# Kernel optimization log

Measured on AMD Instinct MI355X. Metric: run time of the kernel, lower is better.

Reference implementation:

```python
import jax, jax.numpy as jnp
import numpy as np

B, S, D = 2, 512, 1024
H, DH = 16, 64
P, K, F = 16, 4, 4096
EPS = 1e-6


def setup_inputs() -> dict:
    key = jax.random.key(0)
    ks = jax.random.split(key, 9)
    sc = D ** -0.5
    return {
        "x": jax.random.normal(ks[0], (B, S, D), jnp.float32),
        "wq": jax.random.normal(ks[1], (D, D), jnp.float32) * sc,
        "wk": jax.random.normal(ks[2], (D, D), jnp.float32) * sc,
        "wv": jax.random.normal(ks[3], (D, D), jnp.float32) * sc,
        "wo": jax.random.normal(ks[4], (D, D), jnp.float32) * sc,
        "g1": jnp.ones((D,), jnp.float32),
        "g2": jnp.ones((D,), jnp.float32),
        "r1": jax.random.normal(ks[5], (D, P), jnp.float32) * sc,
        "r2": jax.random.normal(ks[6], (D, P), jnp.float32) * sc,
        "bank1": jax.random.normal(ks[7], (P, D, F), jnp.float32) * 0.02,
        "bank2": jax.random.normal(ks[8], (P, F, D), jnp.float32) * 0.02,
    }


def _rmsnorm(t, g):
    return t * jax.lax.rsqrt(jnp.mean(t * t, axis=-1, keepdims=True) + EPS) * g


def reference(x, wq, wk, wv, wo, g1, g2, r1, r2, bank1, bank2):
    # --- attention sublayer (pre-norm, causal SDPA) ---
    h = _rmsnorm(x, g1)
    q = (h @ wq).reshape(B, S, H, DH).transpose(0, 2, 1, 3)  # (B,H,S,DH)
    k = (h @ wk).reshape(B, S, H, DH).transpose(0, 2, 1, 3)
    v = (h @ wv).reshape(B, S, H, DH).transpose(0, 2, 1, 3)
    scores = jnp.einsum("bhqd,bhkd->bhqk", q, k) * (DH ** -0.5)
    causal = jnp.triu(jnp.ones((S, S), bool), k=1)
    scores = jnp.where(causal[None, None], jnp.finfo(scores.dtype).min, scores)
    attn = jax.nn.softmax(scores, axis=-1)
    o = jnp.einsum("bhqk,bhkd->bhqd", attn, v).transpose(0, 2, 1, 3).reshape(B, S, D)
    x = x + o @ wo

    # --- compositional FFN: top-k primitive-bank routing ---
    h = _rmsnorm(x, g2)
    # FC1 routing
    tv1, ti1 = jax.lax.top_k(h @ r1, K)            # (B,S,K)
    c1 = jax.nn.softmax(tv1, axis=-1)
    z1 = jnp.einsum("bsd,pdf->bspf", h, bank1)     # all-primitive FC1 projections
    z1k = jnp.take_along_axis(z1, ti1[..., None], axis=2)  # gather (B,S,K,F)
    hmid = jax.nn.gelu(jnp.einsum("bsk,bskf->bsf", c1, z1k))
    # FC2 routing (same pre-FFN features)
    tv2, ti2 = jax.lax.top_k(h @ r2, K)
    c2 = jax.nn.softmax(tv2, axis=-1)
    z2 = jnp.einsum("bsf,pfd->bspd", hmid, bank2)
    z2k = jnp.take_along_axis(z2, ti2[..., None], axis=2)  # (B,S,K,D)
    ffn_out = jnp.einsum("bsk,bskd->bsd", c2, z2k)
    return x + ffn_out
```

## Files before the change

### kernel.cpp

```cpp
#include <hip/hip_runtime.h>
#include <hip/hip_bf16.h>

#define B_  2
#define S_  512
#define D_  1024
#define H_  16
#define DH_ 64
#define P_  16
#define K_  4
#define F_  4096
#define NT  (B_*S_)
#define EPS_ 1e-6f
#define MT  6

typedef __attribute__((ext_vector_type(8))) short bf16x8s;
typedef __attribute__((ext_vector_type(4))) float f32x4;

__device__ inline unsigned short f2bf(float f) {
    unsigned int u = __builtin_bit_cast(unsigned int, f);
    unsigned int r = (u + 0x7fffu + ((u >> 16) & 1u)) >> 16;
    return (unsigned short)r;
}
__device__ inline float bf2f(unsigned short u) {
    unsigned int x = ((unsigned int)u) << 16;
    return __builtin_bit_cast(float, x);
}

__global__ void rmsnorm_kernel(const float* __restrict__ x, const float* __restrict__ g,
                               float* __restrict__ out, __hip_bfloat16* __restrict__ outbf) {
    int t = blockIdx.x;
    const float* row = x + (size_t)t * D_;
    float ss = 0.f;
    for (int d = threadIdx.x; d < D_; d += 256) { float v = row[d]; ss += v * v; }
    __shared__ float red[4];
    for (int off = 32; off; off >>= 1) ss += __shfl_xor(ss, off);
    int w = threadIdx.x >> 6;
    if ((threadIdx.x & 63) == 0) red[w] = ss;
    __syncthreads();
    if (threadIdx.x == 0) red[0] = rsqrtf((red[0]+red[1]+red[2]+red[3]) / (float)D_ + EPS_);
    __syncthreads();
    float scale = red[0];
    for (int d = threadIdx.x; d < D_; d += 256) {
        float v = row[d] * scale * g[d];
        out[(size_t)t * D_ + d] = v;
        if (outbf) outbf[(size_t)t * D_ + d] = __float2bfloat16(v);
    }
}

template<bool RES>
__device__ __forceinline__
void gemm64_body(const float* __restrict__ A, const float* __restrict__ Bw,
                 const float* __restrict__ Res, float* __restrict__ C,
                 int N, int Kd, int m0, int n0,
                 float (*As)[64], float (*Bs)[64]) {
    int t = threadIdx.x;
    int tx = t & 15, ty = t >> 4;
    float acc[4][4] = {};
    for (int k0 = 0; k0 < Kd; k0 += 16) {
        #pragma unroll
        for (int i = 0; i < 4; i++) {
            int idx = t*4 + i; int m = idx >> 4, kk = idx & 15;
            As[kk][m] = A[(size_t)(m0+m)*Kd + k0 + kk];
        }
        #pragma unroll
        for (int i = 0; i < 4; i++) {
            int idx = t*4 + i; int n = idx & 63, kk = idx >> 6;
            Bs[kk][n] = Bw[(size_t)(k0+kk)*N + n0 + n];
        }
        __syncthreads();
        #pragma unroll
        for (int kk = 0; kk < 16; kk++) {
            float a[4], b[4];
            #pragma unroll
            for (int i = 0; i < 4; i++) a[i] = As[kk][ty*4+i];
            #pragma unroll
            for (int j = 0; j < 4; j++) b[j] = Bs[kk][tx*4+j];
            #pragma unroll
            for (int i = 0; i < 4; i++)
                #pragma unroll
                for (int j = 0; j < 4; j++) acc[i][j] += a[i]*b[j];
        }
        __syncthreads();
    }
    #pragma unroll
    for (int i = 0; i < 4; i++)
        #pragma unroll
        for (int j = 0; j < 4; j++) {
            int m = m0 + ty*4 + i, n = n0 + tx*4 + j;
            float v = acc[i][j];
            if (RES) v += Res[(size_t)m*N + n];
            C[(size_t)m*N + n] = v;
        }
}

template<bool RES>
__global__ void gemm64(const float* __restrict__ A, const float* __restrict__ Bw,
                       const float* __restrict__ Res, float* __restrict__ C,
                       int M, int N, int Kd) {
    __shared__ float As[16][64];
    __shared__ float Bs[16][64];
    gemm64_body<RES>(A, Bw, Res, C, N, Kd, blockIdx.y*64, blockIdx.x*64, As, Bs);
}

__global__ void qkv64(const float* __restrict__ A, const float* __restrict__ wq,
                      const float* __restrict__ wk, const float* __restrict__ wv,
                      float* __restrict__ qb, float* __restrict__ kb, float* __restrict__ vb) {
    __shared__ float As[16][64];
    __shared__ float Bs[16][64];
    int which = blockIdx.x >> 4;
    const float* Bw = (which == 0) ? wq : (which == 1) ? wk : wv;
    float* C = (which == 0) ? qb : (which == 1) ? kb : vb;
    gemm64_body<false>(A, Bw, nullptr, C, D_, D_, blockIdx.y*64, (blockIdx.x & 15)*64, As, Bs);
}

template<bool SPLIT>
__global__ __launch_bounds__(512)
void attn5(const float* __restrict__ q, const float* __restrict__ k,
           const float* __restrict__ v, float* __restrict__ o,
           float* __restrict__ opart, float* __restrict__ mpart,
           float* __restrict__ lpart) {
    __shared__ float Qs[64][68];
    __shared__ float Ks[64][68];
    __shared__ float Vs[64][68];
    int bh = blockIdx.y;
    int bq0 = (bh >> 4) * S_;
    int hh = bh & 15;
    int qt = blockIdx.x, q0 = qt * 64;
    int z = SPLIT ? blockIdx.z : 0;
    int t = threadIdx.x;
    int tx = t & 15;
    int ry = (t >> 4) & 31;

    #pragma unroll
    for (int i = 0; i < 2; i++) {
        int idx = i*512 + t; int r = idx >> 4, c = idx & 15;
        float4 tmp = *(const float4*)&q[((size_t)(bq0 + q0 + r))*D_ + hh*64 + c*4];
        tmp.x *= 0.125f; tmp.y *= 0.125f; tmp.z *= 0.125f; tmp.w *= 0.125f;
        *(float4*)&Qs[r][c*4] = tmp;
    }
    float m[2], l[2], oacc[2][4];
    #pragma unroll
    for (int i = 0; i < 2; i++) {
        m[i] = -1e30f; l[i] = 0.f;
        #pragma unroll
        for (int jd = 0; jd < 4; jd++) oacc[i][jd] = 0.f;
    }
    __syncthreads();

    for (int kt = z; kt <= qt; kt += (SPLIT ? 2 : 1)) {
        int j0 = kt * 64;
        __syncthreads();
        #pragma unroll
        for (int i = 0; i < 2; i++) {
            int idx = i*512 + t; int r = idx >> 4, c = idx & 15;
            *(float4*)&Ks[r][c*4] = *(const float4*)&k[((size_t)(bq0 + j0 + r))*D_ + hh*64 + c*4];
            *(float4*)&Vs[r][c*4] = *(const float4*)&v[((size_t)(bq0 + j0 + r))*D_ + hh*64 + c*4];
        }
        __syncthreads();

        float sacc[2][4] = {};
        #pragma unroll
        for (int dc = 0; dc < 16; dc++) {
            f32x4 qv[2], kv[4];
            #pragma unroll
            for (int i = 0; i < 2; i++) qv[i] = *(const f32x4*)&Qs[ry + 32*i][dc*4];
            #pragma unroll
            for (int j = 0; j < 4; j++) kv[j] = *(const f32x4*)&Ks[tx + 16*j][dc*4];
            #pragma unroll
            for (int i = 0; i < 2; i++)
                #pragma unroll
                for (int j = 0; j < 4; j++)
                    sacc[i][j] += qv[i][0]*kv[j][0] + qv[i][1]*kv[j][1]
                                + qv[i][2]*kv[j][2] + qv[i][3]*kv[j][3];
        }
        if (kt == qt) {
            #pragma unroll
            for (int i = 0; i < 2; i++)
                #pragma unroll
                for (int j = 0; j < 4; j++)
                    if (tx + 16*j > ry + 32*i) sacc[i][j] = -1e30f;
        }
        #pragma unroll
        for (int i = 0; i < 2; i++) {
            float tm = fmaxf(fmaxf(sacc[i][0], sacc[i][1]), fmaxf(sacc[i][2], sacc[i][3]));
            tm = fmaxf(tm, __shfl_xor(tm, 1));
            tm = fmaxf(tm, __shfl_xor(tm, 2));
            tm = fmaxf(tm, __shfl_xor(tm, 4));
            tm = fmaxf(tm, __shfl_xor(tm, 8));
            float mn = fmaxf(m[i], tm);
            float corr = __expf(m[i] - mn);
            m[i] = mn;
            float rs = 0.f;
            #pragma unroll
            for (int j = 0; j < 4; j++) { sacc[i][j] = __expf(sacc[i][j] - mn); rs += sacc[i][j]; }
            rs += __shfl_xor(rs, 1);
            rs += __shfl_xor(rs, 2);
            rs += __shfl_xor(rs, 4);
            rs += __shfl_xor(rs, 8);
            l[i] = l[i]*corr + rs;
            #pragma unroll
            for (int jd = 0; jd < 4; jd++) oacc[i][jd] *= corr;
        }
        __syncthreads();
        #pragma unroll
        for (int i = 0; i < 2; i++)
            #pragma unroll
            for (int j = 0; j < 4; j++)
                Ks[ry + 32*i][tx + 16*j] = sacc[i][j];
        __syncthreads();
        #pragma unroll
        for (int jc = 0; jc < 16; jc++) {
            f32x4 pv4[2];
            #pragma unroll
            for (int i = 0; i < 2; i++) pv4[i] = *(const f32x4*)&Ks[ry + 32*i][jc*4];
            #pragma unroll
            for (int u = 0; u < 4; u++) {
                int j = jc*4 + u;
                float vv[4];
                #pragma unroll
                for (int jd = 0; jd < 4; jd++) vv[jd] = Vs[j][tx + 16*jd];
                #pragma unroll
                for (int i = 0; i < 2; i++)
                    #pragma unroll
                    for (int jd = 0; jd < 4; jd++) oacc[i][jd] += pv4[i][u] * vv[jd];
            }
        }
    }
    if (SPLIT) {
        int zb = z*32 + bh;
        #pragma unroll
        for (int i = 0; i < 2; i++) {
            int row = q0 + ry + 32*i;
            if (tx == 0) {
                mpart[(size_t)zb*S_ + row] = m[i];
                lpart[(size_t)zb*S_ + row] = l[i];
            }
            #pragma unroll
            for (int jd = 0; jd < 4; jd++)
                opart[((size_t)zb*S_ + row)*64 + tx + 16*jd] = oacc[i][jd];
        }
    } else {
        #pragma unroll
        for (int i = 0; i < 2; i++) {
            float inv = 1.f / l[i];
            #pragma unroll
            for (int jd = 0; jd < 4; jd++)
                o[((size_t)(bq0 + q0 + ry + 32*i))*D_ + hh*64 + tx + 16*jd] = oacc[i][jd] * inv;
        }
    }
}

__global__ void attn_merge(const float* __restrict__ opart, const float* __restrict__ mpart,
                           const float* __restrict__ lpart, float* __restrict__ o) {
    int i = blockIdx.x*256 + threadIdx.x;
    if (i >= 32*S_*16) return;
    int c4 = i & 15, q = (i >> 4) & (S_-1), bh = i >> 13;
    float m0 = mpart[(size_t)bh*S_ + q],      m1 = mpart[(size_t)(32+bh)*S_ + q];
    float l0 = lpart[(size_t)bh*S_ + q],      l1 = lpart[(size_t)(32+bh)*S_ + q];
    float M = fmaxf(m0, m1);
    float w0 = __expf(m0 - M), w1 = __expf(m1 - M);
    float inv = 1.f / (l0*w0 + l1*w1);
    const float4* p0 = (const float4*)(opart + ((size_t)bh*S_ + q)*64);
    const float4* p1 = (const float4*)(opart + ((size_t)(32+bh)*S_ + q)*64);
    float4 a = p0[c4], b = p1[c4];
    float4 r;
    r.x = (a.x*w0 + b.x*w1) * inv;
    r.y = (a.y*w0 + b.y*w1) * inv;
    r.z = (a.z*w0 + b.z*w1) * inv;
    r.w = (a.w*w0 + b.w*w1) * inv;
    int bq0 = (bh >> 4)*S_, hh = bh & 15;
    *(float4*)&o[((size_t)(bq0 + q))*D_ + hh*64 + c4*4] = r;
}

__device__ void topk_write(const float* vals, float* c, int* ti) {
    float v[P_];
    #pragma unroll
    for (int p = 0; p < P_; p++) v[p] = vals[p];
    int idx[K_]; float tv[K_];
    for (int kk = 0; kk < K_; kk++) {
        int bi = 0; float bv = -1e30f;
        for (int p = 0; p < P_; p++) if (v[p] > bv) { bv = v[p]; bi = p; }
        idx[kk] = bi; tv[kk] = bv; v[bi] = -1e30f;
    }
    float mx = tv[0], sum = 0.f, e[K_];
    for (int kk = 0; kk < K_; kk++) { e[kk] = __expf(tv[kk]-mx); sum += e[kk]; }
    for (int kk = 0; kk < K_; kk++) { c[kk] = e[kk]/sum; ti[kk] = idx[kk]; }
}

__global__ void routing_kernel(const float* __restrict__ h, const float* __restrict__ r1,
                               const float* __restrict__ r2,
                               float* c1, int* ti1, float* c2, int* ti2) {
    int t = blockIdx.x; int lane = threadIdx.x;
    float acc1[P_] = {}, acc2[P_] = {};
    for (int d = lane; d < D_; d += 64) {
        float x = h[(size_t)t*D_ + d];
        #pragma unroll
        for (int p = 0; p < P_; p++) {
            acc1[p] += x * r1[d*P_ + p];
            acc2[p] += x * r2[d*P_ + p];
        }
    }
    #pragma unroll
    for (int p = 0; p < P_; p++)
        for (int off = 32; off; off >>= 1) {
            acc1[p] += __shfl_xor(acc1[p], off);
            acc2[p] += __shfl_xor(acc2[p], off);
        }
    if (lane == 0) {
        topk_write(acc1, c1 + t*K_, ti1 + t*K_);
        topk_write(acc2, c2 + t*K_, ti2 + t*K_);
    }
}

__global__ void build_lists(const int* __restrict__ ti1, const int* __restrict__ ti2,
                            int* cnt1, int* list1, int* cnt2, int* list2) {
    int slot = blockIdx.x*256 + threadIdx.x;
    if (slot >= NT*K_) return;
    int p1 = ti1[slot]; int pos1 = atomicAdd(&cnt1[p1], 1); list1[p1*(NT*K_) + pos1] = slot;
    int p2 = ti2[slot]; int pos2 = atomicAdd(&cnt2[p2], 1); list2[p2*(NT*K_) + pos2] = slot;
}

__device__ inline void store_out(__hip_bfloat16* p, float v) { *p = __float2bfloat16(v); }
__device__ inline void store_out(float* p, float v)          { *p = v; }

template<typename OutT, int KSPLIT>
__global__ __launch_bounds__(256)
void mgemm7(const __hip_bfloat16* __restrict__ A, const float* __restrict__ Bw0,
            const int* __restrict__ cnt, const int* __restrict__ list,
            const float* __restrict__ coef,
            OutT* __restrict__ o0, OutT* __restrict__ o1,
            OutT* __restrict__ o2, OutT* __restrict__ o3,
            int Kd, int Nd, int ntn) {
    __shared__ unsigned short Asl[4*128*8];
    __shared__ unsigned short Bsl[4*128*8];
    __shared__ int rows_s[128];
    __shared__ int slots_s[128];
    int p  = blockIdx.x / ntn;
    int n0 = (blockIdx.x - p*ntn) * 128;
    int m0 = blockIdx.y * 128;
    int count = cnt[p];
    if (m0 >= count) return;
    int t = threadIdx.x;
    if (t < 128) {
        int si = m0 + t;
        int slot = (si < count) ? list[p*(NT*K_) + si] : -1;
        slots_s[t] = slot;
        rows_s[t] = (slot >= 0) ? (slot >> 2) : 0;
    }
    __syncthreads();
    const float* Bw = Bw0 + (size_t)p * (size_t)Kd * Nd;
    int z = (KSPLIT > 1) ? (int)blockIdx.z : 0;
    OutT* out = (z == 0) ? o0 : (z == 1) ? o1 : (z == 2) ? o2 : o3;
    int kbase = z * (Kd / KSPLIT);
    int kend  = kbase + Kd / KSPLIT;
    int lane = t & 63, wave = t >> 6;
    int wr = wave >> 1, wc = wave & 1;
    int l15 = lane & 15, l4 = lane >> 4;
    int ar0 = t >> 2, ac8 = t & 3;
    int bkg = t & 7, bcg = t >> 3;
    f32x4 acc[4][4];
    #pragma unroll
    for (int i = 0; i < 4; i++)
        #pragma unroll
        for (int j = 0; j < 4; j++) acc[i][j] = (f32x4){0.f,0.f,0.f,0.f};
    int atok0 = rows_s[ar0], atok1 = rows_s[64 + ar0];
    for (int k0 = kbase; k0 < kend; k0 += 32) {
        __syncthreads();
        {
            bf16x8s av0 = *(const bf16x8s*)&A[(size_t)atok0*Kd + k0 + ac8*8];
            bf16x8s av1 = *(const bf16x8s*)&A[(size_t)atok1*Kd + k0 + ac8*8];
            *(bf16x8s*)&Asl[ac8*1024 + ((ar0 ^ (ac8<<1)) * 8)] = av0;
            *(bf16x8s*)&Asl[ac8*1024 + (((64 + ar0) ^ (ac8<<1)) * 8)] = av1;
        }
        {
            float bvv[4][4];
            #pragma unroll
            for (int j = 0; j < 4; j++) {
                float4 tmp = *(const float4*)&Bw[(size_t)(k0 + bkg*4 + j)*Nd + n0 + bcg*4];
                bvv[j][0]=tmp.x; bvv[j][1]=tmp.y; bvv[j][2]=tmp.z; bvv[j][3]=tmp.w;
            }
            int g = bkg >> 1, ib = (bkg & 1) * 4;
            #pragma unroll
            for (int cc = 0; cc < 4; cc++) {
                int col = bcg*4 + cc;
                ushort4 u = make_ushort4(f2bf(bvv[0][cc]), f2bf(bvv[1][cc]),
                                         f2bf(bvv[2][cc]), f2bf(bvv[3][cc]));
                *(ushort4*)&Bsl[g*1024 + ((col ^ (g<<1)) * 8) + ib] = u;
            }
        }
        __syncthreads();
        bf16x8s af[4], bfr[4];
        #pragma unroll
        for (int m = 0; m < 4; m++) {
            int row = wr*64 + m*16 + l15;
            af[m] = *(const bf16x8s*)&Asl[l4*1024 + ((row ^ (l4<<1)) * 8)];
        }
        #pragma unroll
        for (int n = 0; n < 4; n++) {
            int col = wc*64 + n*16 + l15;
            bfr[n] = *(const bf16x8s*)&Bsl[l4*1024 + ((col ^ (l4<<1)) * 8)];
        }
        #pragma unroll
        for (int m = 0; m < 4; m++)
            #pragma unroll
            for (int n = 0; n < 4; n++)
                acc[m][n] = __builtin_amdgcn_mfma_f32_16x16x32_bf16(af[m], bfr[n], acc[m][n], 0, 0, 0);
    }
    #pragma unroll
    for (int m = 0; m < 4; m++) {
        #pragma unroll
        for (int rr = 0; rr < 4; rr++) {
            int rl = wr*64 + m*16 + l4*4 + rr;
            int slot = slots_s[rl];
            if (slot < 0) continue;
            float cf = coef[slot];
            OutT* orow = out + (size_t)slot*Nd + n0 + wc*64;
            #pragma unroll
            for (int n = 0; n < 4; n++)
                store_out(&orow[n*16 + l15], acc[m][n][rr] * cf);
        }
    }
}

__global__ void reduce_fc1(const __hip_bfloat16* __restrict__ z1k,
                           __hip_bfloat16* __restrict__ hmid) {
    int i = blockIdx.x*256 + threadIdx.x;
    if (i >= NT*(F_/8)) return;
    int t = i / (F_/8), f8 = i - t*(F_/8);
    float s[8];
    #pragma unroll
    for (int e = 0; e < 8; e++) s[e] = 0.f;
    #pragma unroll
    for (int kk = 0; kk < K_; kk++) {
        size_t off = (size_t)(t*K_ + kk)*F_ + f8*8;
        bf16x8s a = *(const bf16x8s*)&z1k[off];
        #pragma unroll
        for (int e = 0; e < 8; e++) s[e] += bf2f((unsigned short)a[e]);
    }
    short r[8];
    #pragma unroll
    for (int e = 0; e < 8; e++) {
        float v = s[e];
        float inner = 0.7978845608028654f * (v + 0.044715f * v*v*v);
        r[e] = (short)f2bf(0.5f * v * (1.f + tanhf(inner)));
    }
    bf16x8s rv;
    #pragma unroll
    for (int e = 0; e < 8; e++) rv[e] = r[e];
    *(bf16x8s*)&hmid[(size_t)t*F_ + f8*8] = rv;
}

__global__ void final8(const float* __restrict__ x2,
                       const __hip_bfloat16* __restrict__ z0,
                       const __hip_bfloat16* __restrict__ z1,
                       const __hip_bfloat16* __restrict__ z2p,
                       const __hip_bfloat16* __restrict__ z3,
                       float* __restrict__ out) {
    int i = blockIdx.x*256 + threadIdx.x;
    if (i >= NT*(D_/8)) return;
    int t = i >> 7, d8 = i & 127;
    size_t base = (size_t)t*D_ + d8*8;
    float4 xa = *(const float4*)&x2[base];
    float4 xb = *(const float4*)&x2[base + 4];
    float s[8] = {xa.x, xa.y, xa.z, xa.w, xb.x, xb.y, xb.z, xb.w};
    #pragma unroll
    for (int kk = 0; kk < K_; kk++) {
        size_t off = (size_t)(t*K_ + kk)*D_ + d8*8;
        bf16x8s a = *(const bf16x8s*)&z0[off];
        bf16x8s b = *(const bf16x8s*)&z1[off];
        bf16x8s c = *(const bf16x8s*)&z2p[off];
        bf16x8s d = *(const bf16x8s*)&z3[off];
        #pragma unroll
        for (int e = 0; e < 8; e++)
            s[e] += bf2f((unsigned short)a[e]) + bf2f((unsigned short)b[e])
                  + bf2f((unsigned short)c[e]) + bf2f((unsigned short)d[e]);
    }
    float4 ra = {s[0], s[1], s[2], s[3]};
    float4 rb = {s[4], s[5], s[6], s[7]};
    *(float4*)&out[base] = ra;
    *(float4*)&out[base + 4] = rb;
}

extern "C" void kernel_launch(void* const* d_in, const int* in_sizes, int n_in,
                              void* d_out, int out_size, void* d_ws, size_t ws_size,
                              hipStream_t stream) {
    const float* x  = (const float*)d_in[0];
    const float* wq = (const float*)d_in[1];
    const float* wk = (const float*)d_in[2];
    const float* wv = (const float*)d_in[3];
    const float* wo = (const float*)d_in[4];
    const float* g1 = (const float*)d_in[5];
    const float* g2 = (const float*)d_in[6];
    const float* r1 = (const float*)d_in[7];
    const float* r2 = (const float*)d_in[8];
    const float* bank1 = (const float*)d_in[9];
    const float* bank2 = (const float*)d_in[10];
    float* out = (float*)d_out;

    char* ws = (char*)d_ws;
    const size_t MB = 1ull << 20;
    float* h1   = (float*)(ws + 0*MB);
    float* qb   = (float*)(ws + 4*MB);
    float* kb   = (float*)(ws + 8*MB);
    float* vb   = (float*)(ws + 12*MB);
    float* ob   = (float*)(ws + 16*MB);
    float* x2   = (float*)(ws + 20*MB);
    float* h2   = (float*)(ws + 24*MB);
    float* c1   = (float*)(ws + 28*MB);
    int*   ti1  = (int*)  (ws + 28*MB + 64*1024);
    float* c2   = (float*)(ws + 28*MB + 128*1024);
    int*   ti2  = (int*)  (ws + 28*MB + 192*1024);
    int*   cnt1 = (int*)  (ws + 28*MB + 256*1024);
    int*   cnt2 = (int*)  (ws + 28*MB + 256*1024 + 64);
    int*   list1= (int*)  (ws + 28*MB + 512*1024);
    int*   list2= (int*)  (ws + 28*MB + 768*1024);
    __hip_bfloat16* h2bf = (__hip_bfloat16*)(ws + 30*MB);
    __hip_bfloat16* z1k  = (__hip_bfloat16*)(ws + 32*MB);
    __hip_bfloat16* hmidbf = (__hip_bfloat16*)(ws + 64*MB);
    __hip_bfloat16* z2b0 = (__hip_bfloat16*)(ws + 72*MB);
    __hip_bfloat16* z2b1 = (__hip_bfloat16*)(ws + 80*MB);
    __hip_bfloat16* z2b2 = (__hip_bfloat16*)(ws + 88*MB);
    __hip_bfloat16* z2b3 = (__hip_bfloat16*)(ws + 96*MB);
    float* opart = (float*)(ws + 112*MB);
    float* mpart = (float*)(ws + 120*MB);
    float* lpart = (float*)(ws + 120*MB + 256*1024);

    bool mid = ws_size >= (size_t)122*MB;

    rmsnorm_kernel<<<NT, 256, 0, stream>>>(x, g1, h1, nullptr);
    qkv64<<<dim3(48, 16), 256, 0, stream>>>(h1, wq, wk, wv, qb, kb, vb);
    if (mid) {
        attn5<true><<<dim3(S_/64, B_*H_, 2), 512, 0, stream>>>(
            qb, kb, vb, nullptr, opart, mpart, lpart);
        attn_merge<<<(32*S_*16)/256, 256, 0, stream>>>(opart, mpart, lpart, ob);
    } else {
        attn5<false><<<dim3(S_/64, B_*H_), 512, 0, stream>>>(
            qb, kb, vb, ob, nullptr, nullptr, nullptr);
    }
    dim3 gg(16, 16);
    gemm64<true><<<gg, 256, 0, stream>>>(ob, wo, x, x2, NT, D_, D_);
    rmsnorm_kernel<<<NT, 256, 0, stream>>>(x2, g2, h2, h2bf);
    routing_kernel<<<NT, 64, 0, stream>>>(h2, r1, r2, c1, ti1, c2, ti2);
    hipMemsetAsync(cnt1, 0, 128, stream);
    build_lists<<<(NT*K_)/256, 256, 0, stream>>>(ti1, ti2, cnt1, list1, cnt2, list2);
    mgemm7<__hip_bfloat16, 1><<<dim3(P_*(F_/128), MT, 1), 256, 0, stream>>>(
        h2bf, bank1, cnt1, list1, c1, z1k, nullptr, nullptr, nullptr, D_, F_, F_/128);
    reduce_fc1<<<(NT*(F_/8))/256, 256, 0, stream>>>(z1k, hmidbf);
    mgemm7<__hip_bfloat16, 4><<<dim3(P_*(D_/128), MT, 4), 256, 0, stream>>>(
        hmidbf, bank2, cnt2, list2, c2, z2b0, z2b1, z2b2, z2b3, F_, D_, D_/128);
    final8<<<(NT*(D_/8))/256, 256, 0, stream>>>(x2, z2b0, z2b1, z2b2, z2b3, out);
}
```

Measured before the change: 570.4 us.

## Enlarge routed grouped GEMM tile to 256 rows with 512-thread blocks

The routed expert GEMM now uses 256-row M tiles and 8 waves per block instead of 128 rows and 4 waves. Each fp32 weight tile is loaded from memory and converted to bf16 once per 256 gathered token rows, which halves redundant B-tile reads and conversions. The A and B shared-memory loaders are remapped to the new thread count. The cost is more padding waste on experts with small token counts, a larger LDS footprint per block, and fewer blocks in the grid.

```diff
diff --git a/kernel.cpp b/kernel.cpp
--- a/kernel.cpp
+++ b/kernel.cpp
@@ -11,7 +11,7 @@
 #define F_  4096
 #define NT  (B_*S_)
 #define EPS_ 1e-6f
-#define MT  6
+#define MT2 3
 
 typedef __attribute__((ext_vector_type(8))) short bf16x8s;
 typedef __attribute__((ext_vector_type(4))) float f32x4;
@@ -324,24 +324,24 @@
 __device__ inline void store_out(float* p, float v)          { *p = v; }
 
 template<typename OutT, int KSPLIT>
-__global__ __launch_bounds__(256)
-void mgemm7(const __hip_bfloat16* __restrict__ A, const float* __restrict__ Bw0,
-            const int* __restrict__ cnt, const int* __restrict__ list,
-            const float* __restrict__ coef,
-            OutT* __restrict__ o0, OutT* __restrict__ o1,
-            OutT* __restrict__ o2, OutT* __restrict__ o3,
-            int Kd, int Nd, int ntn) {
-    __shared__ unsigned short Asl[4*128*8];
+__global__ __launch_bounds__(512)
+void mgemm10(const __hip_bfloat16* __restrict__ A, const float* __restrict__ Bw0,
+             const int* __restrict__ cnt, const int* __restrict__ list,
+             const float* __restrict__ coef,
+             OutT* __restrict__ o0, OutT* __restrict__ o1,
+             OutT* __restrict__ o2, OutT* __restrict__ o3,
+             int Kd, int Nd, int ntn) {
+    __shared__ unsigned short Asl[4*256*8];
     __shared__ unsigned short Bsl[4*128*8];
-    __shared__ int rows_s[128];
-    __shared__ int slots_s[128];
+    __shared__ int rows_s[256];
+    __shared__ int slots_s[256];
     int p  = blockIdx.x / ntn;
     int n0 = (blockIdx.x - p*ntn) * 128;
-    int m0 = blockIdx.y * 128;
+    int m0 = blockIdx.y * 256;
     int count = cnt[p];
     if (m0 >= count) return;
     int t = threadIdx.x;
-    if (t < 128) {
+    if (t < 256) {
         int si = m0 + t;
         int slot = (si < count) ? list[p*(NT*K_) + si] : -1;
         slots_s[t] = slot;
@@ -356,36 +356,34 @@
     int lane = t & 63, wave = t >> 6;
     int wr = wave >> 1, wc = wave & 1;
     int l15 = lane & 15, l4 = lane >> 4;
-    int ar0 = t >> 2, ac8 = t & 3;
-    int bkg = t & 7, bcg = t >> 3;
+    int arow = t & 255;
+    int ag0 = (t >> 8) * 2;
+    int kp = t & 15, bcg = t >> 4;
     f32x4 acc[4][4];
     #pragma unroll
     for (int i = 0; i < 4; i++)
         #pragma unroll
         for (int j = 0; j < 4; j++) acc[i][j] = (f32x4){0.f,0.f,0.f,0.f};
-    int atok0 = rows_s[ar0], atok1 = rows_s[64 + ar0];
+    int atok = rows_s[arow];
     for (int k0 = kbase; k0 < kend; k0 += 32) {
         __syncthreads();
         {
-            bf16x8s av0 = *(const bf16x8s*)&A[(size_t)atok0*Kd + k0 + ac8*8];
-            bf16x8s av1 = *(const bf16x8s*)&A[(size_t)atok1*Kd + k0 + ac8*8];
-            *(bf16x8s*)&Asl[ac8*1024 + ((ar0 ^ (ac8<<1)) * 8)] = av0;
-            *(bf16x8s*)&Asl[ac8*1024 + (((64 + ar0) ^ (ac8<<1)) * 8)] = av1;
+            bf16x8s av0 = *(const bf16x8s*)&A[(size_t)atok*Kd + k0 + ag0*8];
+            bf16x8s av1 = *(const bf16x8s*)&A[(size_t)atok*Kd + k0 + (ag0+1)*8];
+            *(bf16x8s*)&Asl[(size_t)(ag0*256 + (arow ^ (ag0<<1)))*8] = av0;
+            *(bf16x8s*)&Asl[(size_t)((ag0+1)*256 + (arow ^ ((ag0+1)<<1)))*8] = av1;
         }
         {
-            float bvv[4][4];
-            #pragma unroll
-            for (int j = 0; j < 4; j++) {
-                float4 tmp = *(const float4*)&Bw[(size_t)(k0 + bkg*4 + j)*Nd + n0 + bcg*4];
-                bvv[j][0]=tmp.x; bvv[j][1]=tmp.y; bvv[j][2]=tmp.z; bvv[j][3]=tmp.w;
-            }
-            int g = bkg >> 1, ib = (bkg & 1) * 4;
+            float4 b0 = *(const float4*)&Bw[(size_t)(k0 + kp*2    )*Nd + n0 + bcg*4];
+            float4 b1 = *(const float4*)&Bw[(size_t)(k0 + kp*2 + 1)*Nd + n0 + bcg*4];
+            float b0a[4] = {b0.x, b0.y, b0.z, b0.w};
+            float b1a[4] = {b1.x, b1.y, b1.z, b1.w};
+            int g = kp >> 2, i2 = (kp & 3) * 2;
             #pragma unroll
             for (int cc = 0; cc < 4; cc++) {
                 int col = bcg*4 + cc;
-                ushort4 u = make_ushort4(f2bf(bvv[0][cc]), f2bf(bvv[1][cc]),
-                                         f2bf(bvv[2][cc]), f2bf(bvv[3][cc]));
-                *(ushort4*)&Bsl[g*1024 + ((col ^ (g<<1)) * 8) + ib] = u;
+                unsigned int u = (unsigned int)f2bf(b0a[cc]) | ((unsigned int)f2bf(b1a[cc]) << 16);
+                *(unsigned int*)&Bsl[(size_t)(g*128 + (col ^ (g<<1)))*8 + i2] = u;
             }
         }
         __syncthreads();
@@ -393,12 +391,12 @@
         #pragma unroll
         for (int m = 0; m < 4; m++) {
             int row = wr*64 + m*16 + l15;
-            af[m] = *(const bf16x8s*)&Asl[l4*1024 + ((row ^ (l4<<1)) * 8)];
+            af[m] = *(const bf16x8s*)&Asl[(size_t)(l4*256 + (row ^ (l4<<1)))*8];
         }
         #pragma unroll
         for (int n = 0; n < 4; n++) {
             int col = wc*64 + n*16 + l15;
-            bfr[n] = *(const bf16x8s*)&Bsl[l4*1024 + ((col ^ (l4<<1)) * 8)];
+            bfr[n] = *(const bf16x8s*)&Bsl[(size_t)(l4*128 + (col ^ (l4<<1)))*8];
         }
         #pragma unroll
         for (int m = 0; m < 4; m++)
@@ -543,10 +541,10 @@
     routing_kernel<<<NT, 64, 0, stream>>>(h2, r1, r2, c1, ti1, c2, ti2);
     hipMemsetAsync(cnt1, 0, 128, stream);
     build_lists<<<(NT*K_)/256, 256, 0, stream>>>(ti1, ti2, cnt1, list1, cnt2, list2);
-    mgemm7<__hip_bfloat16, 1><<<dim3(P_*(F_/128), MT, 1), 256, 0, stream>>>(
+    mgemm10<__hip_bfloat16, 1><<<dim3(P_*(F_/128), MT2, 1), 512, 0, stream>>>(
         h2bf, bank1, cnt1, list1, c1, z1k, nullptr, nullptr, nullptr, D_, F_, F_/128);
     reduce_fc1<<<(NT*(F_/8))/256, 256, 0, stream>>>(z1k, hmidbf);
-    mgemm7<__hip_bfloat16, 4><<<dim3(P_*(D_/128), MT, 4), 256, 0, stream>>>(
+    mgemm10<__hip_bfloat16, 4><<<dim3(P_*(D_/128), MT2, 4), 512, 0, stream>>>(
         hmidbf, bank2, cnt2, list2, c2, z2b0, z2b1, z2b2, z2b3, F_, D_, D_/128);
     final8<<<(NT*(D_/8))/256, 256, 0, stream>>>(x2, z2b0, z2b1, z2b2, z2b3, out);
 }
```

After: 634.0 us. +11.1%, slower.
